# Kernel optimization log

Measured on AMD Instinct MI355X. Metric: run time of the kernel, lower is better.

Reference implementation:

```python
import jax, jax.numpy as jnp
import numpy as np

E, K, B = 64, 8, 32
IN_DIM, OUT_DIM = 1024, 1024


def setup_inputs() -> dict:
    key = jax.random.key(0)
    k1, k2, k3, k4, k5, k6 = jax.random.split(key, 6)
    return {
        "weight_probs": jax.random.uniform(k1, (B, K), dtype=jnp.float32),
        "bias_probs": jax.random.uniform(k2, (B, K), dtype=jnp.float32),
        "weight_indices": jax.random.randint(k3, (B, K), 0, E, dtype=jnp.int64),
        "bias_indices": jax.random.randint(k4, (B, K), 0, E, dtype=jnp.int64),
        # parameter banks: one linear layer's params per expert
        "weight_bank": jax.random.normal(k5, (E, OUT_DIM, IN_DIM), dtype=jnp.float32) * 0.02,
        "bias_bank": jax.random.normal(k6, (E, OUT_DIM), dtype=jnp.float32) * 0.02,
    }


def reference(weight_probs, bias_probs, weight_indices, bias_indices, weight_bank, bias_bank):
    # _select_parameters: gather per-(batch, top_k) expert params
    sel_w = weight_bank[weight_indices]          # [B, K, O, I]
    sel_b = bias_bank[bias_indices]              # [B, K, O]
    # _compute_mixture: probability-weighted sum over the top_k axis
    weight_mixture = jnp.einsum("bk,bkoi->boi", weight_probs, sel_w)  # [B, O, I]
    bias_mixture = jnp.einsum("bk,bko->bo", bias_probs, sel_b)        # [B, O]
    return weight_mixture, bias_mixture
```

## Files before the change

### kernel.cpp

```cpp
#include <hip/hip_runtime.h>
#include <hip/hip_bf16.h>


typedef __attribute__((ext_vector_type(8)))  short short8v;
typedef __attribute__((ext_vector_type(16))) float f32x16;
typedef __attribute__((ext_vector_type(4)))  float float4v;

constexpr int E = 64;
constexpr int K = 8;
constexpr int B = 32;
constexpr int OUT_DIM = 1024;

constexpr int NCOL     = 1024 * 1024;
constexpr int BLK      = 256;
constexpr int GRID     = 512;
constexpr int WAVES    = GRID * 4;
constexpr int CPW      = NCOL / WAVES;
constexpr int CSTEP    = 128;
constexpr int STEPS    = CPW / CSTEP;
constexpr int NRG      = STEPS * 4;
constexpr int WM_ELEMS = B * NCOL;
constexpr int OB4      = OUT_DIM / 4;

struct HL { short h; short l; };

__device__ __forceinline__ HL split_bf16(float x) {
    const __hip_bfloat16 hb = __float2bfloat16(x);
    const float          hf = __bfloat162float(hb);
    const __hip_bfloat16 lb = __float2bfloat16(x - hf);
    HL r;
    r.h = __builtin_bit_cast(short, hb);
    r.l = __builtin_bit_cast(short, lb);
    return r;
}

__global__ __launch_bounds__(BLK, 2) void ParameterMixture_86835648790543_kernel(
    const float* __restrict__ wprobs,
    const float* __restrict__ bprobs,
    const int*   __restrict__ widx,
    const int*   __restrict__ bidx,
    const float* __restrict__ wbank,
    const float* __restrict__ bbank,
    float*       __restrict__ out)
{
    const int bid  = blockIdx.x;
    const int t    = threadIdx.x;
    const int wv   = t >> 6;
    const int lane = t & 63;
    const int m    = lane & 31;
    const int kh   = (lane >> 5) * 8;
    const int cl   = lane & 31;

    if (bid < 32) {
        const int tt   = bid * BLK + t;
        const int b    = tt / OB4;
        const int off4 = tt % OB4;
        const float4* __restrict__ bb4 = (const float4*)bbank;
        float4 a4 = make_float4(0.f, 0.f, 0.f, 0.f);
#pragma unroll
        for (int k = 0; k < K; ++k) {
            const float p = bprobs[b * K + k];
            const int   e = bidx[b * K + k];
            const float4 v = bb4[e * OB4 + off4];
            a4.x += p * v.x; a4.y += p * v.y;
            a4.z += p * v.z; a4.w += p * v.w;
        }
        ((float4*)(out + WM_ELEMS))[tt] = a4;
    }

    float wp[K];
    int   wi[K];
#pragma unroll
    for (int k2 = 0; k2 < K; ++k2) {
        wp[k2] = wprobs[m * K + k2];
        wi[k2] = widx[m * K + k2];
    }
    short8v aH[4], aL[4];
#pragma unroll
    for (int s = 0; s < 4; ++s) {
#pragma unroll
        for (int j = 0; j < 8; ++j) {
            const int e = s * 16 + kh + j;
            float p = 0.f;
#pragma unroll
            for (int k2 = 0; k2 < K; ++k2)
                p += (wi[k2] == e) ? wp[k2] : 0.f;
            const HL r = split_bf16(p);
            aH[s][j] = r.h;
            aL[s][j] = r.l;
        }
    }

    const size_t ncol     = (size_t)NCOL;
    const int    wave_id  = bid * 4 + wv;
    const int    col_base = wave_id * CPW;

    auto load_rg = [&](float4v (&w)[8], int g) {
        if (g > NRG - 1) g = NRG - 1;
        const int c0 = col_base + (g >> 2) * CSTEP + 4 * cl;
        const int r0 = (g & 3) * 16 + kh;
        const float* __restrict__ base = wbank + c0;
#pragma unroll
        for (int j = 0; j < 8; ++j)
            w[j] = __builtin_nontemporal_load(
                (const float4v*)(base + (size_t)(r0 + j) * ncol));
    };

    float4v bufA[8], bufB[8], bufC[8], bufD[8];
    load_rg(bufA, 0);
    load_rg(bufB, 1);
    load_rg(bufC, 2);
    load_rg(bufD, 3);

#pragma unroll 1
    for (int step = 0; step < STEPS; ++step) {
        f32x16 acc[4];
#pragma unroll
        for (int tt2 = 0; tt2 < 4; ++tt2)
#pragma unroll
            for (int i = 0; i < 16; ++i) acc[tt2][i] = 0.f;

        const int g0 = step * 4;

        auto compute_rg = [&](const float4v (&w)[8], int rg) {
            short8v bh[4], bl[4];
#pragma unroll
            for (int j = 0; j < 8; ++j) {
                const HL rx = split_bf16(w[j][0]);
                const HL ry = split_bf16(w[j][1]);
                const HL rz = split_bf16(w[j][2]);
                const HL rw = split_bf16(w[j][3]);
                bh[0][j] = rx.h; bl[0][j] = rx.l;
                bh[1][j] = ry.h; bl[1][j] = ry.l;
                bh[2][j] = rz.h; bl[2][j] = rz.l;
                bh[3][j] = rw.h; bl[3][j] = rw.l;
            }
#pragma unroll
            for (int tt2 = 0; tt2 < 4; ++tt2) {
                acc[tt2] = __builtin_amdgcn_mfma_f32_32x32x16_bf16(aH[rg], bh[tt2], acc[tt2], 0, 0, 0);
                acc[tt2] = __builtin_amdgcn_mfma_f32_32x32x16_bf16(aH[rg], bl[tt2], acc[tt2], 0, 0, 0);
                acc[tt2] = __builtin_amdgcn_mfma_f32_32x32x16_bf16(aL[rg], bh[tt2], acc[tt2], 0, 0, 0);
            }
        };

        compute_rg(bufA, 0);  load_rg(bufA, g0 + 4);
        compute_rg(bufB, 1);  load_rg(bufB, g0 + 5);
        compute_rg(bufC, 2);  load_rg(bufC, g0 + 6);
        compute_rg(bufD, 3);  load_rg(bufD, g0 + 7);

        const int c0 = col_base + step * CSTEP + 4 * cl;
        float* __restrict__ ob = out + c0 + (size_t)((lane >> 5) * 4) * ncol;
#pragma unroll
        for (int reg = 0; reg < 16; ++reg) {
            const int row = (reg & 3) + 8 * (reg >> 2);
            float4v v;
            v[0] = acc[0][reg]; v[1] = acc[1][reg];
            v[2] = acc[2][reg]; v[3] = acc[3][reg];
            __builtin_nontemporal_store(v, (float4v*)(ob + (size_t)row * ncol));
        }
    }
}

extern "C" void kernel_launch(void* const* d_in, const int* in_sizes, int n_in,
                              void* d_out, int out_size, void* d_ws, size_t ws_size,
                              hipStream_t stream) {
    const float* wprobs = (const float*)d_in[0];
    const float* bprobs = (const float*)d_in[1];
    const int*   widx   = (const int*)d_in[2];
    const int*   bidx   = (const int*)d_in[3];
    const float* wbank  = (const float*)d_in[4];
    const float* bbank  = (const float*)d_in[5];
    float*       out    = (float*)d_out;

    ParameterMixture_86835648790543_kernel<<<GRID, BLK, 0, stream>>>(
        wprobs, bprobs, widx, bidx, wbank, bbank, out);
}
```

Measured before the change: 90.67 us.

## Launch one wave per 128-column tile instead of a persistent looping grid

```diff
diff --git a/kernel.cpp b/kernel.cpp
--- a/kernel.cpp
+++ b/kernel.cpp
@@ -13,12 +13,8 @@
 
 constexpr int NCOL     = 1024 * 1024;
 constexpr int BLK      = 256;
-constexpr int GRID     = 512;
-constexpr int WAVES    = GRID * 4;
-constexpr int CPW      = NCOL / WAVES;
-constexpr int CSTEP    = 128;
-constexpr int STEPS    = CPW / CSTEP;
-constexpr int NRG      = STEPS * 4;
+constexpr int CPW      = 128;
+constexpr int GRID     = NCOL / CPW / 4;
 constexpr int WM_ELEMS = B * NCOL;
 constexpr int OB4      = OUT_DIM / 4;
 
@@ -95,69 +91,59 @@
     const int    wave_id  = bid * 4 + wv;
     const int    col_base = wave_id * CPW;
 
-    auto load_rg = [&](float4v (&w)[8], int g) {
-        if (g > NRG - 1) g = NRG - 1;
-        const int c0 = col_base + (g >> 2) * CSTEP + 4 * cl;
-        const int r0 = (g & 3) * 16 + kh;
-        const float* __restrict__ base = wbank + c0;
+    const float* __restrict__ wbase = wbank + col_base + 4 * cl;
+
+    auto load_rg = [&](float4v (&w)[8], int rg) {
+        const int r0 = rg * 16 + kh;
 #pragma unroll
         for (int j = 0; j < 8; ++j)
             w[j] = __builtin_nontemporal_load(
-                (const float4v*)(base + (size_t)(r0 + j) * ncol));
+                (const float4v*)(wbase + (size_t)(r0 + j) * ncol));
     };
 
-    float4v bufA[8], bufB[8], bufC[8], bufD[8];
+    f32x16 acc[4];
+#pragma unroll
+    for (int tt2 = 0; tt2 < 4; ++tt2)
+#pragma unroll
+        for (int i = 0; i < 16; ++i) acc[tt2][i] = 0.f;
+
+    auto compute_rg = [&](const float4v (&w)[8], int rg) {
+        short8v bh[4], bl[4];
+#pragma unroll
+        for (int j = 0; j < 8; ++j) {
+            const HL rx = split_bf16(w[j][0]);
+            const HL ry = split_bf16(w[j][1]);
+            const HL rz = split_bf16(w[j][2]);
+            const HL rw = split_bf16(w[j][3]);
+            bh[0][j] = rx.h; bl[0][j] = rx.l;
+            bh[1][j] = ry.h; bl[1][j] = ry.l;
+            bh[2][j] = rz.h; bl[2][j] = rz.l;
+            bh[3][j] = rw.h; bl[3][j] = rw.l;
+        }
+#pragma unroll
+        for (int tt2 = 0; tt2 < 4; ++tt2) {
+            acc[tt2] = __builtin_amdgcn_mfma_f32_32x32x16_bf16(aH[rg], bh[tt2], acc[tt2], 0, 0, 0);
+            acc[tt2] = __builtin_amdgcn_mfma_f32_32x32x16_bf16(aH[rg], bl[tt2], acc[tt2], 0, 0, 0);
+            acc[tt2] = __builtin_amdgcn_mfma_f32_32x32x16_bf16(aL[rg], bh[tt2], acc[tt2], 0, 0, 0);
+        }
+    };
+
+    float4v bufA[8], bufB[8];
     load_rg(bufA, 0);
     load_rg(bufB, 1);
-    load_rg(bufC, 2);
-    load_rg(bufD, 3);
+    compute_rg(bufA, 0);  load_rg(bufA, 2);
+    compute_rg(bufB, 1);  load_rg(bufB, 3);
+    compute_rg(bufA, 2);
+    compute_rg(bufB, 3);
 
-#pragma unroll 1
-    for (int step = 0; step < STEPS; ++step) {
-        f32x16 acc[4];
+    float* __restrict__ ob = out + col_base + 4 * cl + (size_t)((lane >> 5) * 4) * ncol;
 #pragma unroll
-        for (int tt2 = 0; tt2 < 4; ++tt2)
-#pragma unroll
-            for (int i = 0; i < 16; ++i) acc[tt2][i] = 0.f;
-
-        const int g0 = step * 4;
-
-        auto compute_rg = [&](const float4v (&w)[8], int rg) {
-            short8v bh[4], bl[4];
-#pragma unroll
-            for (int j = 0; j < 8; ++j) {
-                const HL rx = split_bf16(w[j][0]);
-                const HL ry = split_bf16(w[j][1]);
-                const HL rz = split_bf16(w[j][2]);
-                const HL rw = split_bf16(w[j][3]);
-                bh[0][j] = rx.h; bl[0][j] = rx.l;
-                bh[1][j] = ry.h; bl[1][j] = ry.l;
-                bh[2][j] = rz.h; bl[2][j] = rz.l;
-                bh[3][j] = rw.h; bl[3][j] = rw.l;
-            }
-#pragma unroll
-            for (int tt2 = 0; tt2 < 4; ++tt2) {
-                acc[tt2] = __builtin_amdgcn_mfma_f32_32x32x16_bf16(aH[rg], bh[tt2], acc[tt2], 0, 0, 0);
-                acc[tt2] = __builtin_amdgcn_mfma_f32_32x32x16_bf16(aH[rg], bl[tt2], acc[tt2], 0, 0, 0);
-                acc[tt2] = __builtin_amdgcn_mfma_f32_32x32x16_bf16(aL[rg], bh[tt2], acc[tt2], 0, 0, 0);
-            }
-        };
-
-        compute_rg(bufA, 0);  load_rg(bufA, g0 + 4);
-        compute_rg(bufB, 1);  load_rg(bufB, g0 + 5);
-        compute_rg(bufC, 2);  load_rg(bufC, g0 + 6);
-        compute_rg(bufD, 3);  load_rg(bufD, g0 + 7);
-
-        const int c0 = col_base + step * CSTEP + 4 * cl;
-        float* __restrict__ ob = out + c0 + (size_t)((lane >> 5) * 4) * ncol;
-#pragma unroll
-        for (int reg = 0; reg < 16; ++reg) {
-            const int row = (reg & 3) + 8 * (reg >> 2);
-            float4v v;
-            v[0] = acc[0][reg]; v[1] = acc[1][reg];
-            v[2] = acc[2][reg]; v[3] = acc[3][reg];
-            __builtin_nontemporal_store(v, (float4v*)(ob + (size_t)row * ncol));
-        }
+    for (int reg = 0; reg < 16; ++reg) {
+        const int row = (reg & 3) + 8 * (reg >> 2);
+        float4v v;
+        v[0] = acc[0][reg]; v[1] = acc[1][reg];
+        v[2] = acc[2][reg]; v[3] = acc[3][reg];
+        __builtin_nontemporal_store(v, (float4v*)(ob + (size_t)row * ncol));
     }
 }
 
```

Result: slower. 98.04 us (+8.1%).
